# Kernel optimization log

Measured on AMD Instinct MI355X. Metric: run time of the kernel, lower is better.

Reference implementation:

```python
import jax, jax.numpy as jnp
import numpy as np

B, N, D, K, L, H, DFF = 2048, 64, 256, 32, 2, 8, 1024
TEMP = 10.0
EPS = 1e-10


def _ln(x, g, b):
    m = jnp.mean(x, -1, keepdims=True)
    v = jnp.mean((x - m) ** 2, -1, keepdims=True)
    return (x - m) * jax.lax.rsqrt(v + 1e-5) * g + b


def _mha(x, Wqkv, bqkv, Wo, bo):
    b, n, d = x.shape
    dh = d // H
    qkv = x @ Wqkv.T + bqkv                      # [b,n,3d]
    q, k, v = jnp.split(qkv, 3, axis=-1)
    q = q.reshape(b, n, H, dh)
    k = k.reshape(b, n, H, dh)
    v = v.reshape(b, n, H, dh)
    att = jnp.einsum('bqhd,bkhd->bhqk', q, k) / np.float32(np.sqrt(dh))
    att = jax.nn.softmax(att, axis=-1)
    o = jnp.einsum('bhqk,bkhd->bqhd', att, v).reshape(b, n, d)
    return o @ Wo.T + bo


def _encoder(x, Wqkv, bqkv, Wo, bo, ln1_g, ln1_b, ln2_g, ln2_b, W1, b1, W2, b2):
    # torch TransformerEncoder, norm_first=False (post-LN), dropout=0
    for l in range(L):
        x = _ln(x + _mha(x, Wqkv[l], bqkv[l], Wo[l], bo[l]), ln1_g[l], ln1_b[l])
        h = jax.nn.relu(x @ W1[l].T + b1[l]) @ W2[l].T + b2[l]
        x = _ln(x + h, ln2_g[l], ln2_b[l])
    return x


def _cluster_probs_from_emb(emb, mus):
    # ||x - tanh(mu)||^2 via expansion to avoid the [B,N,K,D] intermediate
    mt = jnp.tanh(mus)                                       # [K,D]
    d2 = (jnp.sum(emb ** 2, -1)[..., None]
          - 2.0 * jnp.einsum('bnd,kd->bnk', emb, mt)
          + jnp.sum(mt ** 2, -1))                            # [B,N,K]
    e = jnp.exp(-d2 / TEMP)
    return e / jnp.sum(e, -1, keepdims=True)


def _forward(input_series, init_logits, transition_logits,
             Wqkv, bqkv, Wo, bo, ln1_g, ln1_b, ln2_g, ln2_b,
             W1, b1, W2, b2, mus):
    prob_pi = jax.nn.softmax(init_logits, axis=0)            # [K]
    prob_A = jax.nn.softmax(transition_logits, axis=1)       # [K,K]
    emb_all = _encoder(input_series, Wqkv, bqkv, Wo, bo,
                       ln1_g, ln1_b, ln2_g, ln2_b, W1, b1, W2, b2)
    logits_all = _cluster_probs_from_emb(emb_all, mus)       # [B,N,K]

    log_emit = jnp.log(logits_all + EPS)                     # [B,N,K]
    lt0 = jax.nn.softmax(jnp.log(prob_pi + EPS)[None, :] + log_emit[:, 0], axis=1)

    def step(lt, le):
        lt = jax.nn.softmax(jnp.log(lt @ prob_A + EPS) + le, axis=1)
        return lt, lt

    _, rest = jax.lax.scan(step, lt0, jnp.swapaxes(log_emit[:, 1:], 0, 1))
    cluster_probs = jnp.concatenate([lt0[:, None], jnp.swapaxes(rest, 0, 1)], axis=1)
    entropy_loss = -jnp.mean(jnp.sum(cluster_probs * jnp.log(cluster_probs + EPS), -1))
    return cluster_probs, emb_all, prob_pi, prob_A, entropy_loss


def setup_inputs() -> dict:
    key = jax.random.key(0)
    ks = jax.random.split(key, 10)
    s = jnp.float32(0.02)
    return {
        'input_series': jax.random.normal(ks[0], (B, N, D), jnp.float32),
        'init_logits': jax.random.normal(ks[1], (K,), jnp.float32),
        'transition_logits': jax.random.normal(ks[2], (K, K), jnp.float32),
        'Wqkv': jax.random.normal(ks[3], (L, 3 * D, D), jnp.float32) * s,
        'bqkv': jnp.zeros((L, 3 * D), jnp.float32),
        'Wo': jax.random.normal(ks[4], (L, D, D), jnp.float32) * s,
        'bo': jnp.zeros((L, D), jnp.float32),
        'ln1_g': jnp.ones((L, D), jnp.float32),
        'ln1_b': jnp.zeros((L, D), jnp.float32),
        'ln2_g': jnp.ones((L, D), jnp.float32),
        'ln2_b': jnp.zeros((L, D), jnp.float32),
        'W1': jax.random.normal(ks[5], (L, DFF, D), jnp.float32) * s,
        'b1': jnp.zeros((L, DFF), jnp.float32),
        'W2': jax.random.normal(ks[6], (L, D, DFF), jnp.float32) * s,
        'b2': jnp.zeros((L, D), jnp.float32),
        'mus': jax.random.normal(ks[7], (K, D), jnp.float32),
    }


def reference(input_series, init_logits, transition_logits, Wqkv, bqkv, Wo, bo,
              ln1_g, ln1_b, ln2_g, ln2_b, W1, b1, W2, b2, mus):
    return _forward(input_series, init_logits, transition_logits, Wqkv, bqkv,
                    Wo, bo, ln1_g, ln1_b, ln2_g, ln2_b, W1, b1, W2, b2, mus)
```

## Files before the change

kernel.cpp:

```cpp
#include <hip/hip_runtime.h>

#define BB   2048
#define NNX  64
#define DD   256
#define KKC  32
#define LLN  2
#define HHN  8
#define DHH  32
#define DFFN 1024
#define BNT  (BB*NNX)

typedef short s16x8 __attribute__((ext_vector_type(8)));
typedef float f32x4 __attribute__((ext_vector_type(4)));

#define GLOAD_LDS16(gp, lp) __builtin_amdgcn_global_load_lds( \
    (const __attribute__((address_space(1))) void*)(gp),      \
    (__attribute__((address_space(3))) void*)(lp), 16, 0, 0)

#define WAITVM4() asm volatile("s_waitcnt vmcnt(4)" ::: "memory")
#define WAITVM0() asm volatile("s_waitcnt vmcnt(0)" ::: "memory")
#define SBAR() __builtin_amdgcn_s_barrier()

__device__ __forceinline__ unsigned short f2bf(float f) {
  unsigned int u = __float_as_uint(f);
  u += 0x7fffu + ((u >> 16) & 1u);
  return (unsigned short)(u >> 16);
}
__device__ __forceinline__ float bf2f(unsigned short u) {
  return __uint_as_float(((unsigned int)u) << 16);
}

__global__ __launch_bounds__(256) void cvt_kernel(const float4* __restrict__ src,
                                                  ushort4* __restrict__ dst, int n4) {
  int i = blockIdx.x * 256 + threadIdx.x;
  int st = gridDim.x * 256;
  for (; i < n4; i += st) {
    float4 v = src[i];
    ushort4 o;
    o.x = f2bf(v.x); o.y = f2bf(v.y); o.z = f2bf(v.z); o.w = f2bf(v.w);
    dst[i] = o;
  }
}

__global__ void mt_kernel(const float* __restrict__ mus, float* __restrict__ mtT,
                          float* __restrict__ mtn) {
  int k = threadIdx.x;
  if (k < 32) {
    float acc = 0.f;
    for (int d = 0; d < 256; d++) {
      float t = tanhf(mus[k * 256 + d]);
      mtT[d * 32 + k] = t;
      acc += t * t;
    }
    mtn[k] = acc;
  }
}

__global__ void piA_kernel(const float* __restrict__ il, const float* __restrict__ tl,
                           float* __restrict__ d_pi, float* __restrict__ d_A,
                           float* __restrict__ d_ent) {
  int lane = threadIdx.x;
  if (lane == 0) *d_ent = 0.f;
  if (lane < 32) {
    float v = il[lane];
    float mx = v;
    #pragma unroll
    for (int off = 16; off; off >>= 1) mx = fmaxf(mx, __shfl_xor(mx, off, 32));
    float e = expf(v - mx), sm = e;
    #pragma unroll
    for (int off = 16; off; off >>= 1) sm += __shfl_xor(sm, off, 32);
    d_pi[lane] = e / sm;
    for (int r = 0; r < 32; r++) {
      float a = tl[r * 32 + lane];
      float m2 = a;
      #pragma unroll
      for (int off = 16; off; off >>= 1) m2 = fmaxf(m2, __shfl_xor(m2, off, 32));
      float e2 = expf(a - m2), s2 = e2;
      #pragma unroll
      for (int off = 16; off; off >>= 1) s2 += __shfl_xor(s2, off, 32);
      d_A[r * 32 + lane] = e2 / s2;
    }
  }
}

template <int EPI>
__global__ __launch_bounds__(256, 4) void gemm_nt(const unsigned short* __restrict__ A,
                                                  const unsigned short* __restrict__ Bw,
                                                  const float* __restrict__ bias,
                                                  unsigned short* __restrict__ outp,
                                                  int N, int K, int nx) {
  __shared__ unsigned short lds[16384];
  const int t = threadIdx.x;
  const int bid = blockIdx.x, nwg = gridDim.x;
  const int wg = (bid & 7) * (nwg >> 3) + (bid >> 3);
  const int m0 = (wg / nx) << 7;
  const int n0 = (wg % nx) << 7;
  const int lane = t & 63, w = t >> 6;
  const int wm = w >> 1, wn = w & 1;
  const int lr = lane & 15, lk = lane >> 4;

  const int r0 = t >> 2, sg = t & 3;
  const int s0 = sg ^ ((r0 >> 1) & 3);
  const int r1 = r0 + 64;
  const int s1 = sg ^ ((r1 >> 1) & 3);
  const int aoff0 = (m0 + r0) * K + s0 * 8;
  const int aoff1 = (m0 + r1) * K + s1 * 8;
  const int boff0 = (n0 + r0) * K + s0 * 8;
  const int boff1 = (n0 + r1) * K + s1 * 8;

#define STAGE(buf, k0) do {                                    \
    char* la = (char*)lds + (buf) * 16384;                     \
    GLOAD_LDS16(A + aoff0 + (k0), la + t * 16);                \
    GLOAD_LDS16(A + aoff1 + (k0), la + 4096 + t * 16);         \
    GLOAD_LDS16(Bw + boff0 + (k0), la + 8192 + t * 16);        \
    GLOAD_LDS16(Bw + boff1 + (k0), la + 12288 + t * 16);       \
  } while (0)

  f32x4 acc[4][4];
  #pragma unroll
  for (int i = 0; i < 4; i++)
    #pragma unroll
    for (int j = 0; j < 4; j++) acc[i][j] = (f32x4)(0.f);

  const int ra = wm * 64 + lr, rb = wn * 64 + lr;
  const int sla = lk ^ ((ra >> 1) & 3), slb = lk ^ ((rb >> 1) & 3);

  const int NT = K >> 5;
  STAGE(0, 0);
  STAGE(1, 32);
  WAITVM4();
  SBAR();

  int c = 0;
  for (int kt = 0; kt < NT; kt++) {
    s16x8 af[4], bf[4];
    {
      const unsigned short* ua = lds + c * 8192;
      const unsigned short* ub = ua + 4096;
      #pragma unroll
      for (int mf = 0; mf < 4; mf++)
        af[mf] = *(const s16x8*)&ua[(ra + mf * 16) * 32 + sla * 8];
      #pragma unroll
      for (int nf = 0; nf < 4; nf++)
        bf[nf] = *(const s16x8*)&ub[(rb + nf * 16) * 32 + slb * 8];
    }
    __builtin_amdgcn_s_setprio(1);
    #pragma unroll
    for (int mf = 0; mf < 4; mf++)
      #pragma unroll
      for (int nf = 0; nf < 4; nf++)
        acc[mf][nf] = __builtin_amdgcn_mfma_f32_16x16x32_bf16(af[mf], bf[nf], acc[mf][nf], 0, 0, 0);
    __builtin_amdgcn_s_setprio(0);
    SBAR();
    if (kt < NT - 2) {
      STAGE(c, (kt + 2) << 5);
      WAITVM4();
    } else if (kt == NT - 2) {
      WAITVM0();
    }
    SBAR();
    c ^= 1;
  }
#undef STAGE

  #pragma unroll
  for (int nf = 0; nf < 4; nf++) {
    int col = n0 + wn * 64 + nf * 16 + lr;
    float bv = bias[col];
    #pragma unroll
    for (int mf = 0; mf < 4; mf++)
      #pragma unroll
      for (int r = 0; r < 4; r++) {
        int row = m0 + wm * 64 + mf * 16 + lk * 4 + r;
        float v = acc[mf][nf][r] + bv;
        if (EPI == 1) v = fmaxf(v, 0.f);
        outp[(size_t)row * N + col] = f2bf(v);
      }
  }
}

template <bool WR32>
__global__ __launch_bounds__(512) void gemm_ln(const unsigned short* __restrict__ A,
                                               const unsigned short* __restrict__ Bw,
                                               const float* __restrict__ bias,
                                               const unsigned short* __restrict__ res,
                                               const float* __restrict__ g,
                                               const float* __restrict__ bta,
                                               unsigned short* __restrict__ xb,
                                               float* __restrict__ x32,
                                               int K) {
  __shared__ unsigned short As[128 * 64];
  __shared__ unsigned short Bs[256 * 64];
  __shared__ float stats[2][128][4];
  const int t = threadIdx.x;
  const int nwg = gridDim.x;
  const int bid = blockIdx.x;
  const int wg = (bid & 7) * (nwg >> 3) + (bid >> 3);
  const int m0 = wg << 7;

  const int lane = t & 63, w = t >> 6;
  const int wm = w >> 2, wn = w & 3;
  const int lr = lane & 15, lk = lane >> 4;

  size_t aoff[2], boff[4];
  #pragma unroll
  for (int p = 0; p < 2; p++) {
    int u = p * 512 + t;
    int row = u >> 3, sp = u & 7;
    int seg = sp ^ (((row >> 2) & 1) << 1);
    aoff[p] = (size_t)(m0 + row) * K + seg * 8;
  }
  #pragma unroll
  for (int p = 0; p < 4; p++) {
    int u = p * 512 + t;
    int row = u >> 3, sp = u & 7;
    int seg = sp ^ (((row >> 2) & 1) << 1);
    boff[p] = (size_t)row * K + seg * 8;
  }

  f32x4 acc[4][4];
  #pragma unroll
  for (int i = 0; i < 4; i++)
    #pragma unroll
    for (int j = 0; j < 4; j++) acc[i][j] = (f32x4)(0.f);

  for (int k0 = 0; k0 < K; k0 += 64) {
    #pragma unroll
    for (int p = 0; p < 2; p++)
      GLOAD_LDS16(A + aoff[p] + k0, (char*)As + (p * 512 + t) * 16);
    #pragma unroll
    for (int p = 0; p < 4; p++)
      GLOAD_LDS16(Bw + boff[p] + k0, (char*)Bs + (p * 512 + t) * 16);
    __syncthreads();
    #pragma unroll
    for (int z = 0; z < 2; z++) {
      s16x8 af[4], bfr[4];
      #pragma unroll
      for (int mf = 0; mf < 4; mf++) {
        int row = wm * 64 + mf * 16 + lr;
        int cc = (z * 4 + lk) ^ (((row >> 2) & 1) << 1);
        af[mf] = *(const s16x8*)&As[row * 64 + cc * 8];
      }
      #pragma unroll
      for (int nf = 0; nf < 4; nf++) {
        int row = wn * 64 + nf * 16 + lr;
        int cc = (z * 4 + lk) ^ (((row >> 2) & 1) << 1);
        bfr[nf] = *(const s16x8*)&Bs[row * 64 + cc * 8];
      }
      #pragma unroll
      for (int mf = 0; mf < 4; mf++)
        #pragma unroll
        for (int nf = 0; nf < 4; nf++)
          acc[mf][nf] = __builtin_amdgcn_mfma_f32_16x16x32_bf16(af[mf], bfr[nf], acc[mf][nf], 0, 0, 0);
    }
    __syncthreads();
  }

  float bv[4];
  #pragma unroll
  for (int nf = 0; nf < 4; nf++) bv[nf] = bias[wn * 64 + nf * 16 + lr];

  #pragma unroll
  for (int mf = 0; mf < 4; mf++) {
    #pragma unroll
    for (int r = 0; r < 4; r++) {
      int grow = m0 + wm * 64 + mf * 16 + lk * 4 + r;
      float s = 0.f, q = 0.f;
      #pragma unroll
      for (int nf = 0; nf < 4; nf++) {
        int col = wn * 64 + nf * 16 + lr;
        float v = acc[mf][nf][r] + bv[nf] + bf2f(res[(size_t)grow * 256 + col]);
        acc[mf][nf][r] = v;
        s += v; q += v * v;
      }
      #pragma unroll
      for (int off = 1; off < 16; off <<= 1) { s += __shfl_xor(s, off); q += __shfl_xor(q, off); }
      if (lr == 0) {
        int lrow = wm * 64 + mf * 16 + lk * 4 + r;
        stats[0][lrow][wn] = s;
        stats[1][lrow][wn] = q;
      }
    }
  }
  __syncthreads();

  float gv[4], bbv[4];
  #pragma unroll
  for (int nf = 0; nf < 4; nf++) {
    int col = wn * 64 + nf * 16 + lr;
    gv[nf] = g[col]; bbv[nf] = bta[col];
  }
  #pragma unroll
  for (int mf = 0; mf < 4; mf++) {
    #pragma unroll
    for (int r = 0; r < 4; r++) {
      int lrow = wm * 64 + mf * 16 + lk * 4 + r;
      int grow = m0 + lrow;
      float s4 = stats[0][lrow][0] + stats[0][lrow][1] + stats[0][lrow][2] + stats[0][lrow][3];
      float q4 = stats[1][lrow][0] + stats[1][lrow][1] + stats[1][lrow][2] + stats[1][lrow][3];
      float mean = s4 * (1.f / 256.f);
      float var = q4 * (1.f / 256.f) - mean * mean;
      float rs = rsqrtf(var + 1e-5f);
      #pragma unroll
      for (int nf = 0; nf < 4; nf++) {
        int col = wn * 64 + nf * 16 + lr;
        float val = (acc[mf][nf][r] - mean) * rs * gv[nf] + bbv[nf];
        xb[(size_t)grow * 256 + col] = f2bf(val);
        if (WR32) x32[(size_t)grow * 256 + col] = val;
      }
    }
  }
}

__global__ __launch_bounds__(64) void attn_kernel(const unsigned short* __restrict__ qkv,
                                                  unsigned short* __restrict__ ob) {
  __shared__ unsigned short al[6656];
  unsigned short* qs = al;
  unsigned short* ks = al + 2048;
  unsigned short* ps = al;
  unsigned short* vs = al + 4608;
  const int bh = blockIdx.x;
  const int b = bh >> 3, h = bh & 7;
  const int lane = threadIdx.x;
  const int lr = lane & 15, lk = lane >> 4;

  #pragma unroll
  for (int p = 0; p < 4; p++) {
    int u = lane + p * 64;
    int row = u >> 2, seg = u & 3;
    size_t gb = (size_t)(b * 64 + row) * 768 + h * 32 + seg * 8;
    GLOAD_LDS16(qkv + gb, (char*)al + u * 16);
    GLOAD_LDS16(qkv + gb + 256, (char*)al + 4096 + u * 16);
    GLOAD_LDS16(qkv + gb + 512, (char*)al + 9216 + u * 16);
  }
  __syncthreads();

  f32x4 s[4][4];
  #pragma unroll
  for (int i = 0; i < 4; i++)
    #pragma unroll
    for (int j = 0; j < 4; j++) s[i][j] = (f32x4)(0.f);
  s16x8 aq[4], bk[4];
  #pragma unroll
  for (int mi = 0; mi < 4; mi++) aq[mi] = *(const s16x8*)&qs[(mi * 16 + lr) * 32 + lk * 8];
  #pragma unroll
  for (int nj = 0; nj < 4; nj++) bk[nj] = *(const s16x8*)&ks[(nj * 16 + lr) * 32 + lk * 8];
  #pragma unroll
  for (int mi = 0; mi < 4; mi++)
    #pragma unroll
    for (int nj = 0; nj < 4; nj++)
      s[mi][nj] = __builtin_amdgcn_mfma_f32_16x16x32_bf16(aq[mi], bk[nj], s[mi][nj], 0, 0, 0);

  const float scale = 0.17677669529663687f;
  #pragma unroll
  for (int mi = 0; mi < 4; mi++) {
    #pragma unroll
    for (int r = 0; r < 4; r++) {
      float t0 = s[mi][0][r] * scale, t1 = s[mi][1][r] * scale;
      float t2 = s[mi][2][r] * scale, t3 = s[mi][3][r] * scale;
      float mx = fmaxf(fmaxf(t0, t1), fmaxf(t2, t3));
      #pragma unroll
      for (int off = 8; off; off >>= 1) mx = fmaxf(mx, __shfl_xor(mx, off, 16));
      float e0 = expf(t0 - mx), e1 = expf(t1 - mx), e2 = expf(t2 - mx), e3 = expf(t3 - mx);
      float sm = e0 + e1 + e2 + e3;
      #pragma unroll
      for (int off = 8; off; off >>= 1) sm += __shfl_xor(sm, off, 16);
      float inv = 1.f / sm;
      int prow = mi * 16 + lk * 4 + r;
      ps[prow * 72 + lr + 0]  = f2bf(e0 * inv);
      ps[prow * 72 + lr + 16] = f2bf(e1 * inv);
      ps[prow * 72 + lr + 32] = f2bf(e2 * inv);
      ps[prow * 72 + lr + 48] = f2bf(e3 * inv);
    }
  }
  __syncthreads();

  f32x4 oacc[4][2];
  #pragma unroll
  for (int i = 0; i < 4; i++) { oacc[i][0] = (f32x4)(0.f); oacc[i][1] = (f32x4)(0.f); }
  #pragma unroll
  for (int kk = 0; kk < 2; kk++) {
    s16x8 bv[2];
    #pragma unroll
    for (int nf = 0; nf < 2; nf++) {
      s16x8 tmp;
      #pragma unroll
      for (int jj = 0; jj < 8; jj++)
        tmp[jj] = (short)vs[(kk * 32 + lk * 8 + jj) * 32 + nf * 16 + lr];
      bv[nf] = tmp;
    }
    #pragma unroll
    for (int mi = 0; mi < 4; mi++) {
      s16x8 ap = *(const s16x8*)&ps[(mi * 16 + lr) * 72 + kk * 32 + lk * 8];
      #pragma unroll
      for (int nf = 0; nf < 2; nf++)
        oacc[mi][nf] = __builtin_amdgcn_mfma_f32_16x16x32_bf16(ap, bv[nf], oacc[mi][nf], 0, 0, 0);
    }
  }
  #pragma unroll
  for (int mi = 0; mi < 4; mi++)
    #pragma unroll
    for (int nf = 0; nf < 2; nf++)
      #pragma unroll
      for (int r = 0; r < 4; r++) {
        int tok = mi * 16 + lk * 4 + r;
        int c = nf * 16 + lr;
        ob[(size_t)(b * 64 + tok) * 256 + h * 32 + c] = f2bf(oacc[mi][nf][r]);
      }
}

__global__ __launch_bounds__(256) void cluster_kernel(const float* __restrict__ x,
                                                      const float* __restrict__ mtT,
                                                      const float* __restrict__ mtn,
                                                      float* __restrict__ log_emit) {
  __shared__ float mts[8192];
  __shared__ float es[4][256];
  const int t = threadIdx.x;
  #pragma unroll
  for (int i = 0; i < 8; i++)
    ((float4*)mts)[i * 256 + t] = ((const float4*)mtT)[i * 256 + t];
  const int w = t >> 6, lane = t & 63;
  const int k = lane & 31, half = lane >> 5;
  const float mtnr = mtn[k];
  __syncthreads();
  #pragma unroll 1
  for (int it = 0; it < 8; it++) {
    size_t tok = (size_t)blockIdx.x * 32 + (size_t)w * 8 + it;
    float4 u = *((const float4*)(x + tok * 256) + lane);
    *(float4*)&es[w][lane * 4] = u;
    float e2 = u.x * u.x + u.y * u.y + u.z * u.z + u.w * u.w;
    #pragma unroll
    for (int off = 1; off < 64; off <<= 1) e2 += __shfl_xor(e2, off);
    float acc = 0.f;
    const float* ep = &es[w][half * 128];
    const float* mp = &mts[half * 128 * 32 + k];
    #pragma unroll
    for (int d = 0; d < 128; d += 4) {
      float4 ev = *(const float4*)(ep + d);
      acc += ev.x * mp[(d + 0) * 32] + ev.y * mp[(d + 1) * 32]
           + ev.z * mp[(d + 2) * 32] + ev.w * mp[(d + 3) * 32];
    }
    acc += __shfl_xor(acc, 32);
    float d2 = e2 - 2.f * acc + mtnr;
    float e = expf(-d2 * 0.1f);
    float sm = e;
    #pragma unroll
    for (int off = 16; off; off >>= 1) sm += __shfl_xor(sm, off, 32);
    if (half == 0) log_emit[tok * 32 + k] = logf(e / sm + 1e-10f);
  }
}

__global__ __launch_bounds__(256) void scan_kernel(const float* __restrict__ log_emit,
                                                   const float* __restrict__ pi,
                                                   const float* __restrict__ A,
                                                   float* __restrict__ cp,
                                                   float* __restrict__ ent) {
  const int g = threadIdx.x >> 5, j = threadIdx.x & 31;
  const int batch = blockIdx.x * 8 + g;
  float regA[32];
  #pragma unroll
  for (int i = 0; i < 32; i++) regA[i] = A[i * 32 + j];
  const float* le = log_emit + (size_t)batch * 64 * 32;
  float* cpo = cp + (size_t)batch * 64 * 32;

  float u = logf(pi[j] + 1e-10f) + le[j];
  float mx = u;
  #pragma unroll
  for (int off = 16; off; off >>= 1) mx = fmaxf(mx, __shfl_xor(mx, off, 32));
  float e = expf(u - mx), sm = e;
  #pragma unroll
  for (int off = 16; off; off >>= 1) sm += __shfl_xor(sm, off, 32);
  float p = e / sm;
  cpo[j] = p;
  float enta = p * logf(p + 1e-10f);

  for (int n = 1; n < 64; n++) {
    float tt = 0.f;
    #pragma unroll
    for (int i = 0; i < 32; i++) tt += __shfl(p, i, 32) * regA[i];
    u = logf(tt + 1e-10f) + le[n * 32 + j];
    mx = u;
    #pragma unroll
    for (int off = 16; off; off >>= 1) mx = fmaxf(mx, __shfl_xor(mx, off, 32));
    e = expf(u - mx); sm = e;
    #pragma unroll
    for (int off = 16; off; off >>= 1) sm += __shfl_xor(sm, off, 32);
    p = e / sm;
    cpo[n * 32 + j] = p;
    enta += p * logf(p + 1e-10f);
  }
  #pragma unroll
  for (int off = 16; off; off >>= 1) enta += __shfl_xor(enta, off, 32);
  if (j == 0) atomicAdd(ent, -enta * (1.f / (2048.f * 64.f)));
}

extern "C" void kernel_launch(void* const* d_in, const int* in_sizes, int n_in,
                              void* d_out, int out_size, void* d_ws, size_t ws_size,
                              hipStream_t stream) {
  const float* input = (const float*)d_in[0];
  const float* init_logits = (const float*)d_in[1];
  const float* trans = (const float*)d_in[2];
  const float* Wqkv = (const float*)d_in[3];
  const float* bqkv = (const float*)d_in[4];
  const float* Wo = (const float*)d_in[5];
  const float* bo = (const float*)d_in[6];
  const float* ln1g = (const float*)d_in[7];
  const float* ln1b = (const float*)d_in[8];
  const float* ln2g = (const float*)d_in[9];
  const float* ln2b = (const float*)d_in[10];
  const float* W1 = (const float*)d_in[11];
  const float* b1 = (const float*)d_in[12];
  const float* W2 = (const float*)d_in[13];
  const float* b2 = (const float*)d_in[14];
  const float* mus = (const float*)d_in[15];

  float* out = (float*)d_out;
  float* cp = out;
  float* x = out + 4194304;
  float* d_pi = out + 37748736;
  float* d_A = out + 37748768;
  float* d_ent = out + 37749792;

  char* ws = (char*)d_ws;
  unsigned short* qkv = (unsigned short*)ws;
  unsigned short* hb = (unsigned short*)ws;
  float* log_emit = (float*)ws;
  unsigned short* ob = (unsigned short*)(ws + 268435456ull);
  unsigned short* xb = (unsigned short*)(ws + 335544320ull);
  unsigned short* wq_b = (unsigned short*)(ws + 402653184ull);
  unsigned short* wo_b = (unsigned short*)(ws + 402653184ull + 786432ull);
  unsigned short* w1_b = (unsigned short*)(ws + 402653184ull + 1048576ull);
  unsigned short* w2_b = (unsigned short*)(ws + 402653184ull + 2097152ull);
  float* mtT = (float*)(ws + 402653184ull + 3145728ull);
  float* mtn = (float*)(ws + 402653184ull + 3178496ull);

  cvt_kernel<<<2048, 256, 0, stream>>>((const float4*)input, (ushort4*)xb, BNT * 256 / 4);
  cvt_kernel<<<256, 256, 0, stream>>>((const float4*)Wqkv, (ushort4*)wq_b, LLN * 768 * 256 / 4);
  cvt_kernel<<<256, 256, 0, stream>>>((const float4*)Wo, (ushort4*)wo_b, LLN * 256 * 256 / 4);
  cvt_kernel<<<256, 256, 0, stream>>>((const float4*)W1, (ushort4*)w1_b, LLN * 1024 * 256 / 4);
  cvt_kernel<<<256, 256, 0, stream>>>((const float4*)W2, (ushort4*)w2_b, LLN * 256 * 1024 / 4);
  mt_kernel<<<1, 64, 0, stream>>>(mus, mtT, mtn);
  piA_kernel<<<1, 64, 0, stream>>>(init_logits, trans, d_pi, d_A, d_ent);

  for (int l = 0; l < 2; l++) {
    gemm_nt<0><<<6144, 256, 0, stream>>>(xb, wq_b + l * 196608, bqkv + l * 768,
                                         qkv, 768, 256, 6);
    attn_kernel<<<16384, 64, 0, stream>>>(qkv, ob);
    gemm_ln<false><<<1024, 512, 0, stream>>>(ob, wo_b + l * 65536, bo + l * 256,
                                             xb, ln1g + l * 256, ln1b + l * 256,
                                             xb, nullptr, 256);
    gemm_nt<1><<<8192, 256, 0, stream>>>(xb, w1_b + l * 262144, b1 + l * 1024,
                                         hb, 1024, 256, 8);
    if (l == LLN - 1)
      gemm_ln<true><<<1024, 512, 0, stream>>>(hb, w2_b + l * 262144, b2 + l * 256,
                                              xb, ln2g + l * 256, ln2b + l * 256,
                                              xb, x, 1024);
    else
      gemm_ln<false><<<1024, 512, 0, stream>>>(hb, w2_b + l * 262144, b2 + l * 256,
                                               xb, ln2g + l * 256, ln2b + l * 256,
                                               xb, nullptr, 1024);
  }

  cluster_kernel<<<4096, 256, 0, stream>>>(x, mtT, mtn, log_emit);
  scan_kernel<<<256, 256, 0, stream>>>(log_emit, d_pi, d_A, cp, d_ent);
}
```

Before: 1.215 ms.

## Transpose V in LDS for attention, merge weight conversions, read bf16 in cluster

The attention kernel now transposes V into a padded LDS buffer, so the PV MFMA B-operands come from vector loads instead of eight scalar strided reads. It also replaces a block barrier with an LDS wait, which is valid only because the block is a single wavefront. The four weight-conversion launches are merged into one kernel. The cluster kernel now reads the bf16 final activations instead of fp32, which halves its input traffic at some precision cost.

```diff
diff --git a/kernel.cpp b/kernel.cpp
--- a/kernel.cpp
+++ b/kernel.cpp
@@ -19,6 +19,8 @@
 
 #define WAITVM4() asm volatile("s_waitcnt vmcnt(4)" ::: "memory")
 #define WAITVM0() asm volatile("s_waitcnt vmcnt(0)" ::: "memory")
+#define WAITLGKM0() do { asm volatile("s_waitcnt lgkmcnt(0)" ::: "memory"); \
+                         __builtin_amdgcn_sched_barrier(0); } while (0)
 #define SBAR() __builtin_amdgcn_s_barrier()
 
 __device__ __forceinline__ unsigned short f2bf(float f) {
@@ -39,6 +41,26 @@
     ushort4 o;
     o.x = f2bf(v.x); o.y = f2bf(v.y); o.z = f2bf(v.z); o.w = f2bf(v.w);
     dst[i] = o;
+  }
+}
+
+__global__ __launch_bounds__(256) void cvtw_kernel(const float4* __restrict__ wq, ushort4* __restrict__ dq,
+                                                   const float4* __restrict__ wo, ushort4* __restrict__ dov,
+                                                   const float4* __restrict__ w1, ushort4* __restrict__ d1,
+                                                   const float4* __restrict__ w2, ushort4* __restrict__ d2) {
+  const int n0 = 98304, n1 = 32768, n2 = 131072, n3 = 131072;
+  int i = blockIdx.x * 256 + threadIdx.x;
+  int st = gridDim.x * 256;
+  for (; i < n0 + n1 + n2 + n3; i += st) {
+    const float4* s; ushort4* d; int j = i;
+    if (j < n0) { s = wq; d = dq; }
+    else if ((j -= n0) < n1) { s = wo; d = dov; }
+    else if ((j -= n1) < n2) { s = w1; d = d1; }
+    else { j -= n2; s = w2; d = d2; }
+    float4 v = s[j];
+    ushort4 o;
+    o.x = f2bf(v.x); o.y = f2bf(v.y); o.z = f2bf(v.z); o.w = f2bf(v.w);
+    d[j] = o;
   }
 }
 
@@ -314,11 +336,12 @@
 
 __global__ __launch_bounds__(64) void attn_kernel(const unsigned short* __restrict__ qkv,
                                                   unsigned short* __restrict__ ob) {
-  __shared__ unsigned short al[6656];
+  __shared__ unsigned short al[6784];
   unsigned short* qs = al;
   unsigned short* ks = al + 2048;
-  unsigned short* ps = al;
   unsigned short* vs = al + 4608;
+  unsigned short* vt = al;
+  unsigned short* ps = al + 2176;
   const int bh = blockIdx.x;
   const int b = bh >> 3, h = bh & 7;
   const int lane = threadIdx.x;
@@ -335,16 +358,28 @@
   }
   __syncthreads();
 
+  s16x8 aq[4], bk[4], vchunk[4];
+  #pragma unroll
+  for (int mi = 0; mi < 4; mi++) aq[mi] = *(const s16x8*)&qs[(mi * 16 + lr) * 32 + lk * 8];
+  #pragma unroll
+  for (int nj = 0; nj < 4; nj++) bk[nj] = *(const s16x8*)&ks[(nj * 16 + lr) * 32 + lk * 8];
+  const int vrow = lane >> 2, vcs = (lane & 3) * 8;
+  #pragma unroll
+  for (int q = 0; q < 4; q++)
+    vchunk[q] = *(const s16x8*)&vs[(q * 16 + vrow) * 32 + vcs];
+  WAITLGKM0();
+
+  #pragma unroll
+  for (int q = 0; q < 4; q++)
+    #pragma unroll
+    for (int j = 0; j < 8; j++)
+      vt[(vcs + j) * 68 + q * 16 + vrow] = (unsigned short)vchunk[q][j];
+
   f32x4 s[4][4];
   #pragma unroll
   for (int i = 0; i < 4; i++)
     #pragma unroll
     for (int j = 0; j < 4; j++) s[i][j] = (f32x4)(0.f);
-  s16x8 aq[4], bk[4];
-  #pragma unroll
-  for (int mi = 0; mi < 4; mi++) aq[mi] = *(const s16x8*)&qs[(mi * 16 + lr) * 32 + lk * 8];
-  #pragma unroll
-  for (int nj = 0; nj < 4; nj++) bk[nj] = *(const s16x8*)&ks[(nj * 16 + lr) * 32 + lk * 8];
   #pragma unroll
   for (int mi = 0; mi < 4; mi++)
     #pragma unroll
@@ -373,7 +408,7 @@
       ps[prow * 72 + lr + 48] = f2bf(e3 * inv);
     }
   }
-  __syncthreads();
+  WAITLGKM0();
 
   f32x4 oacc[4][2];
   #pragma unroll
@@ -382,13 +417,8 @@
   for (int kk = 0; kk < 2; kk++) {
     s16x8 bv[2];
     #pragma unroll
-    for (int nf = 0; nf < 2; nf++) {
-      s16x8 tmp;
-      #pragma unroll
-      for (int jj = 0; jj < 8; jj++)
-        tmp[jj] = (short)vs[(kk * 32 + lk * 8 + jj) * 32 + nf * 16 + lr];
-      bv[nf] = tmp;
-    }
+    for (int nf = 0; nf < 2; nf++)
+      bv[nf] = *(const s16x8*)&vt[(nf * 16 + lr) * 68 + kk * 32 + lk * 8];
     #pragma unroll
     for (int mi = 0; mi < 4; mi++) {
       s16x8 ap = *(const s16x8*)&ps[(mi * 16 + lr) * 72 + kk * 32 + lk * 8];
@@ -409,7 +439,7 @@
       }
 }
 
-__global__ __launch_bounds__(256) void cluster_kernel(const float* __restrict__ x,
+__global__ __launch_bounds__(256) void cluster_kernel(const unsigned short* __restrict__ xb,
                                                       const float* __restrict__ mtT,
                                                       const float* __restrict__ mtn,
                                                       float* __restrict__ log_emit) {
@@ -426,9 +456,11 @@
   #pragma unroll 1
   for (int it = 0; it < 8; it++) {
     size_t tok = (size_t)blockIdx.x * 32 + (size_t)w * 8 + it;
-    float4 u = *((const float4*)(x + tok * 256) + lane);
-    *(float4*)&es[w][lane * 4] = u;
-    float e2 = u.x * u.x + u.y * u.y + u.z * u.z + u.w * u.w;
+    ushort4 u = *((const ushort4*)(xb + tok * 256) + lane);
+    float v0 = bf2f(u.x), v1 = bf2f(u.y), v2 = bf2f(u.z), v3 = bf2f(u.w);
+    float4 fv = {v0, v1, v2, v3};
+    *(float4*)&es[w][lane * 4] = fv;
+    float e2 = v0 * v0 + v1 * v1 + v2 * v2 + v3 * v3;
     #pragma unroll
     for (int off = 1; off < 64; off <<= 1) e2 += __shfl_xor(e2, off);
     float acc = 0.f;
@@ -535,10 +567,10 @@
   float* mtn = (float*)(ws + 402653184ull + 3178496ull);
 
   cvt_kernel<<<2048, 256, 0, stream>>>((const float4*)input, (ushort4*)xb, BNT * 256 / 4);
-  cvt_kernel<<<256, 256, 0, stream>>>((const float4*)Wqkv, (ushort4*)wq_b, LLN * 768 * 256 / 4);
-  cvt_kernel<<<256, 256, 0, stream>>>((const float4*)Wo, (ushort4*)wo_b, LLN * 256 * 256 / 4);
-  cvt_kernel<<<256, 256, 0, stream>>>((const float4*)W1, (ushort4*)w1_b, LLN * 1024 * 256 / 4);
-  cvt_kernel<<<256, 256, 0, stream>>>((const float4*)W2, (ushort4*)w2_b, LLN * 256 * 1024 / 4);
+  cvtw_kernel<<<512, 256, 0, stream>>>((const float4*)Wqkv, (ushort4*)wq_b,
+                                       (const float4*)Wo, (ushort4*)wo_b,
+                                       (const float4*)W1, (ushort4*)w1_b,
+                                       (const float4*)W2, (ushort4*)w2_b);
   mt_kernel<<<1, 64, 0, stream>>>(mus, mtT, mtn);
   piA_kernel<<<1, 64, 0, stream>>>(init_logits, trans, d_pi, d_A, d_ent);
 
@@ -561,6 +593,6 @@
                                                xb, nullptr, 1024);
   }
 
-  cluster_kernel<<<4096, 256, 0, stream>>>(x, mtT, mtn, log_emit);
+  cluster_kernel<<<4096, 256, 0, stream>>>(xb, mtT, mtn, log_emit);
   scan_kernel<<<256, 256, 0, stream>>>(log_emit, d_pi, d_A, cp, d_ent);
 }
```

Measured after the change: 1.192 ms. No clear change (-1.9%).
